# Kernel optimization log

Hardware: AMD Instinct MI355X
Metric: run time of the kernel (lower is better)

## Reference

```python
import jax, jax.numpy as jnp
import numpy as np

BETA = 0.02  # soft-argmax temperature (CATs / matchsplat default)


def _resize_bilinear_ac(x, out_h, out_w):
    """Bilinear resize over the last two dims, align_corners=True (matches F.interpolate)."""
    H, W = x.shape[-2], x.shape[-1]
    ys = jnp.linspace(0.0, H - 1.0, out_h)
    xs = jnp.linspace(0.0, W - 1.0, out_w)
    y0 = jnp.floor(ys).astype(jnp.int32)
    y1 = jnp.minimum(y0 + 1, H - 1)
    x0 = jnp.floor(xs).astype(jnp.int32)
    x1 = jnp.minimum(x0 + 1, W - 1)
    wy = (ys - y0).astype(x.dtype)
    wx = (xs - x0).astype(x.dtype)
    rows = x[..., y0, :] * (1.0 - wy)[:, None] + x[..., y1, :] * wy[:, None]
    return rows[..., x0] * (1.0 - wx) + rows[..., x1] * wx


def _correlation(f0, f1):
    # f0, f1: [B, C, H, W] -> dense 4D cost volume [B, H0, W0, H1, W1], scaled by 1/sqrt(C)
    b, c, h, w = f0.shape
    return jnp.einsum('bchw,bcuv->bhwuv', f0, f1) / (c ** 0.5)


def _interpolate4d(x, size):
    # x: [B, ch, h1, w1, h2, w2]; separable bilinear over (h2,w2) then (h1,w1), align_corners=True
    B, ch, h1, w1, h2, w2 = x.shape
    x = _resize_bilinear_ac(x.reshape(B, ch * h1 * w1, h2, w2), size[2], size[3])
    x = x.reshape(B, ch, h1, w1, size[2], size[3])
    x = jnp.transpose(x, (0, 1, 4, 5, 2, 3)).reshape(B, ch * size[2] * size[3], h1, w1)
    x = _resize_bilinear_ac(x, size[0], size[1])
    x = x.reshape(B, ch, size[2], size[3], size[0], size[1])
    return jnp.transpose(x, (0, 1, 4, 5, 2, 3))


def _soft_argmax(corr):
    # corr: [B, Hs*Ws, Ht, Wt]; softmax over source positions per target pixel,
    # then marginal expectations of normalized [-1,1] coordinates.
    b, c, h, w = corr.shape
    prob = jax.nn.softmax(corr / BETA, axis=1).reshape(b, h, w, h, w)
    x_normal = jnp.linspace(-1.0, 1.0, w, dtype=corr.dtype)
    y_normal = jnp.linspace(-1.0, 1.0, h, dtype=corr.dtype)
    grid_x = (prob.sum(axis=1) * x_normal[None, :, None, None]).sum(axis=1)[:, None]  # [B,1,h,w]
    grid_y = (prob.sum(axis=2) * y_normal[None, :, None, None]).sum(axis=1)[:, None]
    return grid_x, grid_y


def _mapping_to_flow(mapping):
    # mapping: [B,2,H,W] normalized coords in [-1,1] -> pixel-space flow (map - identity grid)
    B, _, H, W = mapping.shape
    mx = (mapping[:, 0] + 1.0) * (W - 1) / 2.0
    my = (mapping[:, 1] + 1.0) * (H - 1) / 2.0
    gx = jnp.arange(W, dtype=mapping.dtype)[None, :]
    gy = jnp.arange(H, dtype=mapping.dtype)[:, None]
    return jnp.stack([mx - gx, my - gy], axis=1)


def _forward(feat0_c, feat1_c, feat0_f, feat1_f):
    B = feat0_c.shape[0]
    S = 64
    corr_c = _correlation(feat0_c, feat1_c)                        # [B,32,32,32,32]
    corr_c = _interpolate4d(corr_c[:, None], (S, S, S, S))[:, 0]   # [B,64,64,64,64]
    corr_f = _correlation(feat0_f, feat1_f)                        # [B,64,64,64,64]
    c = ((corr_c + corr_f) * 0.5)[:, None]                         # [B,1,64,64,64,64]
    c_flip = jnp.transpose(c, (0, 1, 4, 5, 2, 3))
    gx, gy = _soft_argmax(c_flip.reshape(B, S * S, S, S))
    flow = _mapping_to_flow(jnp.concatenate([gx, gy], axis=1))
    gxf, gyf = _soft_argmax(c.reshape(B, S * S, S, S))
    flow_flip = _mapping_to_flow(jnp.concatenate([gxf, gyf], axis=1))
    trans_features = jnp.stack([feat0_f, feat1_f], axis=1)         # [B,2,C,64,64]
    tc = jnp.stack([feat0_c, feat1_c], axis=1)
    C = tc.shape[2]
    tc = _resize_bilinear_ac(tc.reshape(B * 2, C, tc.shape[-2], tc.shape[-1]), S, S)
    trans_features_coarse = tc.reshape(B, 2, C, S, S)
    return trans_features, trans_features_coarse, c, c_flip, flow, flow_flip


def setup_inputs():
    key = jax.random.key(0)
    k0, k1, k2, k3 = jax.random.split(key, 4)
    B, C = 2, 128
    return {
        'feat0_c': jax.random.normal(k0, (B, C, 32, 32), dtype=jnp.float32),
        'feat1_c': jax.random.normal(k1, (B, C, 32, 32), dtype=jnp.float32),
        'feat0_f': jax.random.normal(k2, (B, C, 64, 64), dtype=jnp.float32),
        'feat1_f': jax.random.normal(k3, (B, C, 64, 64), dtype=jnp.float32),
    }


def reference(feat0_c, feat1_c, feat0_f, feat1_f):
    return _forward(feat0_c, feat1_c, feat0_f, feat1_f)
```

## Files before the change

### kernel.cpp

```cpp
#include <hip/hip_runtime.h>
#include <math.h>

#define SCALE_C 0.08838834764831845f
#define INV_BETA 50.0f
#define STEP63 (2.0f / 63.0f)

__device__ __forceinline__ void interp_coef32(int t, int& i0, int& i1, float& w) {
    float s = (float)(t * 31) / 63.0f;
    i0 = (int)floorf(s);
    if (i0 > 31) i0 = 31;
    i1 = i0 + 1;
    if (i1 > 31) i1 = 31;
    w = s - (float)i0;
}

__global__ __launch_bounds__(256) void k_corr_c(const float* __restrict__ f0c,
                                                const float* __restrict__ f1c,
                                                float* __restrict__ ws) {
    __shared__ float As[16][64];
    __shared__ float Bs[16][64];
    const int b = blockIdx.z;
    const int m0 = blockIdx.y * 64, n0 = blockIdx.x * 64;
    const float* A  = f0c + (long long)b * 131072;
    const float* Bp = f1c + (long long)b * 131072;
    const int tid = threadIdx.x;
    const int tx = tid & 15, ty = tid >> 4;
    const int lk = tid >> 4;
    const int lc = (tid & 15) * 4;
    float acc[4][4] = {{0.f}};
    for (int k0 = 0; k0 < 128; k0 += 16) {
        *(float4*)&As[lk][lc] = *(const float4*)&A[(k0 + lk) * 1024 + m0 + lc];
        *(float4*)&Bs[lk][lc] = *(const float4*)&Bp[(k0 + lk) * 1024 + n0 + lc];
        __syncthreads();
#pragma unroll
        for (int kk = 0; kk < 16; ++kk) {
            float4 a4 = *(float4*)&As[kk][ty * 4];
            float4 b4 = *(float4*)&Bs[kk][tx * 4];
            float av[4] = {a4.x, a4.y, a4.z, a4.w};
            float bv[4] = {b4.x, b4.y, b4.z, b4.w};
#pragma unroll
            for (int i = 0; i < 4; ++i)
#pragma unroll
                for (int j = 0; j < 4; ++j)
                    acc[i][j] = fmaf(av[i], bv[j], acc[i][j]);
        }
        __syncthreads();
    }
#pragma unroll
    for (int i = 0; i < 4; ++i) {
        float4 w4 = make_float4(acc[i][0] * SCALE_C, acc[i][1] * SCALE_C,
                                acc[i][2] * SCALE_C, acc[i][3] * SCALE_C);
        *(float4*)&ws[(long long)b * 1048576 + (long long)(m0 + ty * 4 + i) * 1024 + n0 + tx * 4] = w4;
    }
}

__global__ __launch_bounds__(256, 3) void k_fused2(const float* __restrict__ f0f,
                                                   const float* __restrict__ f1f,
                                                   const float* __restrict__ cws,
                                                   float* __restrict__ c_out,
                                                   float* __restrict__ cf_out,
                                                   float* __restrict__ parts) {
    __shared__ __attribute__((aligned(16))) float smem[12800];
    const int TMP2 = 4096;
    const int b = blockIdx.z, by = blockIdx.y, bx = blockIdx.x;
    const int tid = threadIdx.x;
    const int wv = tid >> 6;
    const int tcl = tid & 7;
    const int trl = (tid >> 3) & 7;
    const int tc = tcl + (wv & 1) * 8;
    const int tr = trl + (wv >> 1) * 8;

    {
        const float* Cc = cws + (long long)b * 1048576;
        for (int e = tid; e < 8192; e += 256) {
            int pair = e >> 11, rem = e & 2047;
            int xc0 = rem >> 6, x1 = rem & 63;
            int s0 = pair >> 1, s1 = pair & 1;
            int ya, yb; float wy0; interp_coef32(2 * by + s0, ya, yb, wy0);
            int za, zb; float wy1; interp_coef32(2 * bx + s1, za, zb, wy1);
            int xa, xb; float wx1; interp_coef32(x1, xa, xb, wx1);
            const float* r0 = Cc + (long long)(ya * 32 + xc0) * 1024;
            const float* r1 = Cc + (long long)(yb * 32 + xc0) * 1024;
            float g0 = (r0[za * 32 + xa] * (1.f - wy1) + r0[zb * 32 + xa] * wy1) * (1.f - wy0)
                     + (r1[za * 32 + xa] * (1.f - wy1) + r1[zb * 32 + xa] * wy1) * wy0;
            float g1 = (r0[za * 32 + xb] * (1.f - wy1) + r0[zb * 32 + xb] * wy1) * (1.f - wy0)
                     + (r1[za * 32 + xb] * (1.f - wy1) + r1[zb * 32 + xb] * wy1) * wy0;
            smem[TMP2 + (pair * 32 + xc0) * 68 + x1] = g0 * (1.f - wx1) + g1 * wx1;
        }
    }

    const float* Ag = f0f + (long long)b * 524288 + by * 128;
    const float* Bg = f1f + (long long)b * 524288 + bx * 128;
    float acc[8][8];
#pragma unroll
    for (int i = 0; i < 8; ++i)
#pragma unroll
        for (int j = 0; j < 8; ++j) acc[i][j] = 0.f;

    for (int ks = 0; ks < 8; ++ks) {
        __syncthreads();
        {
            int v0 = tid, v1 = tid + 256;
            *(float4*)&smem[(v0 >> 5) * 128 + (v0 & 31) * 4] =
                *(const float4*)&Ag[(long long)(ks * 16 + (v0 >> 5)) * 4096 + (v0 & 31) * 4];
            *(float4*)&smem[(v1 >> 5) * 128 + (v1 & 31) * 4] =
                *(const float4*)&Ag[(long long)(ks * 16 + (v1 >> 5)) * 4096 + (v1 & 31) * 4];
            *(float4*)&smem[2048 + (v0 >> 5) * 128 + (v0 & 31) * 4] =
                *(const float4*)&Bg[(long long)(ks * 16 + (v0 >> 5)) * 4096 + (v0 & 31) * 4];
            *(float4*)&smem[2048 + (v1 >> 5) * 128 + (v1 & 31) * 4] =
                *(const float4*)&Bg[(long long)(ks * 16 + (v1 >> 5)) * 4096 + (v1 & 31) * 4];
        }
        __syncthreads();
#pragma unroll
        for (int kk = 0; kk < 16; ++kk) {
            float4 a0 = *(float4*)&smem[kk * 128 + tr * 8];
            float4 a1 = *(float4*)&smem[kk * 128 + tr * 8 + 4];
            float4 b0 = *(float4*)&smem[2048 + kk * 128 + tc * 8];
            float4 b1 = *(float4*)&smem[2048 + kk * 128 + tc * 8 + 4];
            float av[8] = {a0.x, a0.y, a0.z, a0.w, a1.x, a1.y, a1.z, a1.w};
            float bv[8] = {b0.x, b0.y, b0.z, b0.w, b1.x, b1.y, b1.z, b1.w};
#pragma unroll
            for (int i = 0; i < 8; ++i)
#pragma unroll
                for (int j = 0; j < 8; ++j)
                    acc[i][j] = fmaf(av[i], bv[j], acc[i][j]);
        }
    }

    const int pair = wv;
    const int x0b = (tr & 7) * 8, x1b = (tc & 7) * 8;
#pragma unroll
    for (int i = 0; i < 8; ++i) {
        int i0, i1; float w0; interp_coef32(x0b + i, i0, i1, w0);
        float4 ua0 = *(float4*)&smem[TMP2 + (pair * 32 + i0) * 68 + x1b];
        float4 ua1 = *(float4*)&smem[TMP2 + (pair * 32 + i0) * 68 + x1b + 4];
        float4 ub0 = *(float4*)&smem[TMP2 + (pair * 32 + i1) * 68 + x1b];
        float4 ub1 = *(float4*)&smem[TMP2 + (pair * 32 + i1) * 68 + x1b + 4];
        float up[8] = {ua0.x * (1.f - w0) + ub0.x * w0, ua0.y * (1.f - w0) + ub0.y * w0,
                       ua0.z * (1.f - w0) + ub0.z * w0, ua0.w * (1.f - w0) + ub0.w * w0,
                       ua1.x * (1.f - w0) + ub1.x * w0, ua1.y * (1.f - w0) + ub1.y * w0,
                       ua1.z * (1.f - w0) + ub1.z * w0, ua1.w * (1.f - w0) + ub1.w * w0};
#pragma unroll
        for (int j = 0; j < 8; ++j)
            acc[i][j] = (acc[i][j] * SCALE_C + up[j]) * 0.5f;
    }

    {
        long long cb = ((long long)b << 24) + (long long)(by * 128 + tr * 8) * 4096 + bx * 128 + tc * 8;
#pragma unroll
        for (int i = 0; i < 8; ++i) {
            *(float4*)&c_out[cb + (long long)i * 4096] =
                make_float4(acc[i][0], acc[i][1], acc[i][2], acc[i][3]);
            *(float4*)&c_out[cb + (long long)i * 4096 + 4] =
                make_float4(acc[i][4], acc[i][5], acc[i][6], acc[i][7]);
        }
        long long fb = ((long long)b << 24) + (long long)(bx * 128 + tc * 8) * 4096 + by * 128 + tr * 8;
#pragma unroll
        for (int j = 0; j < 8; ++j) {
            *(float4*)&cf_out[fb + (long long)j * 4096] =
                make_float4(acc[0][j], acc[1][j], acc[2][j], acc[3][j]);
            *(float4*)&cf_out[fb + (long long)j * 4096 + 4] =
                make_float4(acc[4][j], acc[5][j], acc[6][j], acc[7][j]);
        }
    }

    float4* pred4 = (float4*)smem;
    float4* parts4 = (float4*)parts;
    __syncthreads();

    {
        float yn1 = -1.f + (float)(2 * bx + (tc >> 3)) * STEP63;
#pragma unroll
        for (int i = 0; i < 8; ++i) {
            float m = acc[i][0];
#pragma unroll
            for (int j = 1; j < 8; ++j) m = fmaxf(m, acc[i][j]);
            m = fmaxf(m, __shfl_xor(m, 1, 64));
            m = fmaxf(m, __shfl_xor(m, 2, 64));
            m = fmaxf(m, __shfl_xor(m, 4, 64));
            float l = 0.f, sx = 0.f;
#pragma unroll
            for (int j = 0; j < 8; ++j) {
                float e = __expf((acc[i][j] - m) * INV_BETA);
                l += e;
                sx += e * (-1.f + (float)(x1b + j) * STEP63);
            }
            l += __shfl_xor(l, 1, 64);  sx += __shfl_xor(sx, 1, 64);
            l += __shfl_xor(l, 2, 64);  sx += __shfl_xor(sx, 2, 64);
            l += __shfl_xor(l, 4, 64);  sx += __shfl_xor(sx, 4, 64);
            if (tcl == 0) pred4[(wv & 1) * 128 + tr * 8 + i] = make_float4(m, l, sx, yn1 * l);
        }
    }
    __syncthreads();
    if (tid < 128) {
        float4 h0 = pred4[tid], h1 = pred4[128 + tid];
        float M = fmaxf(h0.x, h1.x);
        float s0 = __expf((h0.x - M) * INV_BETA);
        float s1 = __expf((h1.x - M) * INV_BETA);
        parts4[((long long)b * 4096 + by * 128 + tid) * 32 + bx] =
            make_float4(M, h0.y * s0 + h1.y * s1, h0.z * s0 + h1.z * s1, h0.w * s0 + h1.w * s1);
    }
    __syncthreads();

    {
        float yn0 = -1.f + (float)(2 * by + (tr >> 3)) * STEP63;
#pragma unroll
        for (int j = 0; j < 8; ++j) {
            float m = acc[0][j];
#pragma unroll
            for (int i = 1; i < 8; ++i) m = fmaxf(m, acc[i][j]);
            m = fmaxf(m, __shfl_xor(m, 8, 64));
            m = fmaxf(m, __shfl_xor(m, 16, 64));
            m = fmaxf(m, __shfl_xor(m, 32, 64));
            float l = 0.f, sx = 0.f;
#pragma unroll
            for (int i = 0; i < 8; ++i) {
                float e = __expf((acc[i][j] - m) * INV_BETA);
                l += e;
                sx += e * (-1.f + (float)(x0b + i) * STEP63);
            }
            l += __shfl_xor(l, 8, 64);   sx += __shfl_xor(sx, 8, 64);
            l += __shfl_xor(l, 16, 64);  sx += __shfl_xor(sx, 16, 64);
            l += __shfl_xor(l, 32, 64);  sx += __shfl_xor(sx, 32, 64);
            if (trl == 0) pred4[(wv >> 1) * 128 + tc * 8 + j] = make_float4(m, l, sx, yn0 * l);
        }
    }
    __syncthreads();
    if (tid < 128) {
        float4 h0 = pred4[tid], h1 = pred4[128 + tid];
        float M = fmaxf(h0.x, h1.x);
        float s0 = __expf((h0.x - M) * INV_BETA);
        float s1 = __expf((h1.x - M) * INV_BETA);
        parts4[262144 + ((long long)b * 4096 + bx * 128 + tid) * 32 + by] =
            make_float4(M, h0.y * s0 + h1.y * s1, h0.z * s0 + h1.z * s1, h0.w * s0 + h1.w * s1);
    }
}

__global__ __launch_bounds__(256) void k_flow(const float* __restrict__ parts,
                                              float* __restrict__ flow,
                                              float* __restrict__ flowf) {
    const int row = blockIdx.x * 4 + (threadIdx.x >> 6);
    const int lane = threadIdx.x & 63;
    const float4* p4 = (const float4*)parts + (long long)row * 32;
    float m = -1e30f, l = 0.f, sx = 0.f, sy = 0.f;
    if (lane < 32) { float4 v = p4[lane]; m = v.x; l = v.y; sx = v.z; sy = v.w; }
    float M = m;
#pragma unroll
    for (int off = 1; off < 64; off <<= 1) M = fmaxf(M, __shfl_xor(M, off, 64));
    float s = __expf((m - M) * INV_BETA);
    l *= s; sx *= s; sy *= s;
#pragma unroll
    for (int off = 1; off < 64; off <<= 1) {
        l += __shfl_xor(l, off, 64);
        sx += __shfl_xor(sx, off, 64);
        sy += __shfl_xor(sy, off, 64);
    }
    if (lane == 0) {
        float gx = sx / l, gy = sy / l;
        float mx = (gx + 1.f) * 31.5f, my = (gy + 1.f) * 31.5f;
        int dir = row >> 13, b = (row >> 12) & 1, p = row & 4095;
        float* o = dir ? flowf : flow;
        o[(long long)b * 8192 + p] = mx - (float)(p & 63);
        o[(long long)b * 8192 + 4096 + p] = my - (float)(p >> 6);
    }
}

__global__ void k_copy_trans(const float* __restrict__ f0f, const float* __restrict__ f1f,
                             float* __restrict__ out1) {
    int idx = blockIdx.x * 256 + threadIdx.x;
    int bv = idx >> 17;
    int r = idx & 131071;
    int b = bv >> 1, v = bv & 1;
    const float4* src = (const float4*)(v ? f1f : f0f) + (long long)b * 131072 + r;
    ((float4*)out1)[idx] = *src;
}

__global__ void k_coarse(const float* __restrict__ f0c, const float* __restrict__ f1c,
                         float* __restrict__ out2) {
    int idx = blockIdx.x * 256 + threadIdx.x;
    int x = idx & 63, y = (idx >> 6) & 63, ch = (idx >> 12) & 127;
    int v = (idx >> 19) & 1, b = idx >> 20;
    int iy0, iy1; float wy; interp_coef32(y, iy0, iy1, wy);
    int ix0, ix1; float wx; interp_coef32(x, ix0, ix1, wx);
    const float* src = (v ? f1c : f0c) + (long long)(b * 128 + ch) * 1024;
    float a  = src[iy0 * 32 + ix0] * (1.f - wy) + src[iy1 * 32 + ix0] * wy;
    float c2 = src[iy0 * 32 + ix1] * (1.f - wy) + src[iy1 * 32 + ix1] * wy;
    out2[idx] = a * (1.f - wx) + c2 * wx;
}

__global__ __launch_bounds__(256) void k_fused_fb(const float* __restrict__ f0f,
                                                  const float* __restrict__ f1f,
                                                  const float* __restrict__ cws,
                                                  float* __restrict__ c_out,
                                                  float* __restrict__ cf_out) {
    __shared__ float As[16][64];
    __shared__ float Bs[16][64];
    __shared__ float tmp[32][33];
    const int b = blockIdx.z, y0 = blockIdx.y, y1 = blockIdx.x;
    const int tid = threadIdx.x;
    const int tx = tid & 15, ty = tid >> 4;
    const float* A  = f0f + (long long)b * 524288 + y0 * 64;
    const float* Bp = f1f + (long long)b * 524288 + y1 * 64;
    int iy0a, iy0b; float wy0; interp_coef32(y0, iy0a, iy0b, wy0);
    int iy1a, iy1b; float wy1; interp_coef32(y1, iy1a, iy1b, wy1);
    const float* Cc = cws + (long long)b * 1048576;
    for (int r = tid; r < 1024; r += 256) {
        int i = r >> 5, j = r & 31;
        const float* ra = Cc + (long long)(iy0a * 32 + i) * 1024;
        const float* rb = Cc + (long long)(iy0b * 32 + i) * 1024;
        float va = ra[iy1a * 32 + j] * (1.f - wy1) + ra[iy1b * 32 + j] * wy1;
        float vb = rb[iy1a * 32 + j] * (1.f - wy1) + rb[iy1b * 32 + j] * wy1;
        tmp[i][j] = va * (1.f - wy0) + vb * wy0;
    }
    float acc[4][4] = {{0.f}};
    const int lk = tid >> 4;
    const int lc = (tid & 15) * 4;
    for (int k0 = 0; k0 < 128; k0 += 16) {
        *(float4*)&As[lk][lc] = *(const float4*)&A[(long long)(k0 + lk) * 4096 + lc];
        *(float4*)&Bs[lk][lc] = *(const float4*)&Bp[(long long)(k0 + lk) * 4096 + lc];
        __syncthreads();
#pragma unroll
        for (int kk = 0; kk < 16; ++kk) {
            float4 a4 = *(float4*)&As[kk][ty * 4];
            float4 b4 = *(float4*)&Bs[kk][tx * 4];
            float av[4] = {a4.x, a4.y, a4.z, a4.w};
            float bv[4] = {b4.x, b4.y, b4.z, b4.w};
#pragma unroll
            for (int i = 0; i < 4; ++i)
#pragma unroll
                for (int j = 0; j < 4; ++j)
                    acc[i][j] = fmaf(av[i], bv[j], acc[i][j]);
        }
        __syncthreads();
    }
    int ix0a[4], ix0b[4]; float wx0[4];
    int ix1a[4], ix1b[4]; float wx1[4];
#pragma unroll
    for (int i = 0; i < 4; ++i) interp_coef32(ty * 4 + i, ix0a[i], ix0b[i], wx0[i]);
#pragma unroll
    for (int j = 0; j < 4; ++j) interp_coef32(tx * 4 + j, ix1a[j], ix1b[j], wx1[j]);
    float val[4][4];
#pragma unroll
    for (int i = 0; i < 4; ++i)
#pragma unroll
        for (int j = 0; j < 4; ++j) {
            float ta = tmp[ix0a[i]][ix1a[j]] * (1.f - wx1[j]) + tmp[ix0a[i]][ix1b[j]] * wx1[j];
            float tb = tmp[ix0b[i]][ix1a[j]] * (1.f - wx1[j]) + tmp[ix0b[i]][ix1b[j]] * wx1[j];
            val[i][j] = (acc[i][j] * SCALE_C + (ta * (1.f - wx0[i]) + tb * wx0[i])) * 0.5f;
        }
    const long long cbase = ((long long)b << 24) + (long long)(y0 * 64) * 4096 + y1 * 64;
#pragma unroll
    for (int i = 0; i < 4; ++i)
        *(float4*)&c_out[cbase + (long long)(ty * 4 + i) * 4096 + tx * 4] =
            make_float4(val[i][0], val[i][1], val[i][2], val[i][3]);
    const long long fbase = ((long long)b << 24) + (long long)(y1 * 64) * 4096 + y0 * 64;
#pragma unroll
    for (int j = 0; j < 4; ++j)
        *(float4*)&cf_out[fbase + (long long)(tx * 4 + j) * 4096 + ty * 4] =
            make_float4(val[0][j], val[1][j], val[2][j], val[3][j]);
}

__global__ __launch_bounds__(256) void k_softargmax(const float* __restrict__ cmat,
                                                    float* __restrict__ flow_out) {
    const int tid = threadIdx.x;
    const float4* src = (const float4*)cmat + (long long)blockIdx.x * 1024;
    float4 r0 = src[tid];
    float4 r1 = src[tid + 256];
    float4 r2 = src[tid + 512];
    float4 r3 = src[tid + 768];
    float m = fmaxf(fmaxf(fmaxf(r0.x, r0.y), fmaxf(r0.z, r0.w)),
                    fmaxf(fmaxf(r1.x, r1.y), fmaxf(r1.z, r1.w)));
    m = fmaxf(m, fmaxf(fmaxf(r2.x, r2.y), fmaxf(r2.z, r2.w)));
    m = fmaxf(m, fmaxf(fmaxf(r3.x, r3.y), fmaxf(r3.z, r3.w)));
    __shared__ float red[16];
    const int lane = tid & 63, wave = tid >> 6;
#pragma unroll
    for (int off = 32; off > 0; off >>= 1) m = fmaxf(m, __shfl_xor(m, off, 64));
    if (lane == 0) red[wave] = m;
    __syncthreads();
    m = fmaxf(fmaxf(red[0], red[1]), fmaxf(red[2], red[3]));
    float l = 0.f, sx = 0.f, sy = 0.f;
#pragma unroll
    for (int s = 0; s < 4; ++s) {
        float4 r = (s == 0) ? r0 : (s == 1) ? r1 : (s == 2) ? r2 : r3;
        int f = tid + s * 256;
        float yn = -1.f + (float)(f >> 4) * STEP63;
        float xb = (float)((f & 15) * 4);
        float e0 = __expf((r.x - m) * 50.f);
        float e1 = __expf((r.y - m) * 50.f);
        float e2 = __expf((r.z - m) * 50.f);
        float e3 = __expf((r.w - m) * 50.f);
        float es = e0 + e1 + e2 + e3;
        l += es;
        sy += es * yn;
        sx += e0 * (-1.f + xb * STEP63) + e1 * (-1.f + (xb + 1.f) * STEP63)
            + e2 * (-1.f + (xb + 2.f) * STEP63) + e3 * (-1.f + (xb + 3.f) * STEP63);
    }
#pragma unroll
    for (int off = 32; off > 0; off >>= 1) {
        l  += __shfl_xor(l, off, 64);
        sx += __shfl_xor(sx, off, 64);
        sy += __shfl_xor(sy, off, 64);
    }
    if (lane == 0) { red[4 + wave] = l; red[8 + wave] = sx; red[12 + wave] = sy; }
    __syncthreads();
    if (tid == 0) {
        float L  = red[4] + red[5] + red[6] + red[7];
        float SX = red[8] + red[9] + red[10] + red[11];
        float SY = red[12] + red[13] + red[14] + red[15];
        float mx = (SX / L + 1.f) * 31.5f;
        float my = (SY / L + 1.f) * 31.5f;
        int bi = blockIdx.x;
        int b = bi >> 12, p = bi & 4095;
        flow_out[(long long)b * 8192 + p]        = mx - (float)(p & 63);
        flow_out[(long long)b * 8192 + 4096 + p] = my - (float)(p >> 6);
    }
}

extern "C" void kernel_launch(void* const* d_in, const int* in_sizes, int n_in,
                              void* d_out, int out_size, void* d_ws, size_t ws_size,
                              hipStream_t stream) {
    const float* f0c = (const float*)d_in[0];
    const float* f1c = (const float*)d_in[1];
    const float* f0f = (const float*)d_in[2];
    const float* f1f = (const float*)d_in[3];
    float* out = (float*)d_out;

    float* c_out  = out + 4194304;
    float* cf_out = out + 37748736;
    float* flow   = out + 71303168;
    float* flowf  = out + 71319552;

    if (ws_size >= (size_t)16777216) {
        float* parts = (float*)d_ws;
        float* cws   = parts + 2097152;
        k_corr_c<<<dim3(16, 16, 2), 256, 0, stream>>>(f0c, f1c, cws);
        k_fused2<<<dim3(32, 32, 2), 256, 0, stream>>>(f0f, f1f, cws, c_out, cf_out, parts);
        k_flow<<<4096, 256, 0, stream>>>(parts, flow, flowf);
        k_copy_trans<<<2048, 256, 0, stream>>>(f0f, f1f, out);
        k_coarse<<<8192, 256, 0, stream>>>(f0c, f1c, out + 2097152);
    } else {
        float* corr_ws = out;
        k_corr_c<<<dim3(16, 16, 2), 256, 0, stream>>>(f0c, f1c, corr_ws);
        k_fused_fb<<<dim3(64, 64, 2), 256, 0, stream>>>(f0f, f1f, corr_ws, c_out, cf_out);
        k_copy_trans<<<2048, 256, 0, stream>>>(f0f, f1f, out);
        k_coarse<<<8192, 256, 0, stream>>>(f0c, f1c, out + 2097152);
        k_softargmax<<<8192, 256, 0, stream>>>(c_out, flow);
        k_softargmax<<<8192, 256, 0, stream>>>(cf_out, flowf);
    }
}
```

Before: 454.1 us.

## Use split-bf16 MFMA for fine correlation GEMM with pre-transposed planes

Adds a pre-pass kernel that splits each fp32 fine feature into high and low bf16 parts and transposes them to pixel-major layout, staged in the output buffer before it is overwritten. The fused correlation kernel then computes the 4096x4096 GEMM with three bf16 MFMA products per tile (hi*hi, lo*hi, hi*lo), loading fragments straight from global memory instead of doing fp32 FMA through shared memory. This moves the dominant compute onto matrix cores at the cost of an extra pass over the fine features and some loss of precision from the bf16x3 approximation. The epilogue, upsampling lookup and soft-argmax reductions are remapped to the MFMA accumulator layout.

```diff
diff --git a/kernel.cpp b/kernel.cpp
--- a/kernel.cpp
+++ b/kernel.cpp
@@ -4,6 +4,9 @@
 #define SCALE_C 0.08838834764831845f
 #define INV_BETA 50.0f
 #define STEP63 (2.0f / 63.0f)
+
+typedef short bf16x8 __attribute__((ext_vector_type(8)));
+typedef float f32x4 __attribute__((ext_vector_type(4)));
 
 __device__ __forceinline__ void interp_coef32(int t, int& i0, int& i1, float& w) {
     float s = (float)(t * 31) / 63.0f;
@@ -54,24 +57,68 @@
     }
 }
 
-__global__ __launch_bounds__(256, 3) void k_fused2(const float* __restrict__ f0f,
-                                                   const float* __restrict__ f1f,
+__global__ __launch_bounds__(256) void k_split(const float* __restrict__ f0f,
+                                               const float* __restrict__ f1f,
+                                               unsigned short* __restrict__ hi,
+                                               unsigned short* __restrict__ lo) {
+    __shared__ unsigned int t[64 * 132];
+    const int m = blockIdx.y;
+    const int pt = blockIdx.x;
+    const float* src = ((m >> 1) ? f1f : f0f) + (size_t)(m & 1) * 524288 + pt * 64;
+    const int tid = threadIdx.x;
+#pragma unroll
+    for (int p = 0; p < 8; ++p) {
+        int k = p * 16 + (tid >> 4);
+        int px = (tid & 15) * 4;
+        float4 v = *(const float4*)&src[(size_t)k * 4096 + px];
+        float vv[4] = {v.x, v.y, v.z, v.w};
+#pragma unroll
+        for (int j = 0; j < 4; ++j) {
+            float x = vv[j];
+            unsigned int u = __float_as_uint(x);
+            unsigned int h = (u + 0x7FFFu + ((u >> 16) & 1u)) >> 16;
+            float r = x - __uint_as_float(h << 16);
+            unsigned int ur = __float_as_uint(r);
+            unsigned int l2 = (ur + 0x7FFFu + ((ur >> 16) & 1u)) >> 16;
+            t[(px + j) * 132 + k] = h | (l2 << 16);
+        }
+    }
+    __syncthreads();
+    const int row = tid >> 2, ks = (tid & 3) * 32;
+    size_t obase = ((size_t)m * 4096 + (size_t)pt * 64 + row) * 128 + ks;
+#pragma unroll
+    for (int c = 0; c < 4; ++c) {
+        unsigned int u[8];
+        *(uint4*)&u[0] = *(const uint4*)&t[row * 132 + ks + c * 8];
+        *(uint4*)&u[4] = *(const uint4*)&t[row * 132 + ks + c * 8 + 4];
+        uint4 ho, lw;
+        ho.x = (u[0] & 0xFFFFu) | (u[1] << 16);
+        ho.y = (u[2] & 0xFFFFu) | (u[3] << 16);
+        ho.z = (u[4] & 0xFFFFu) | (u[5] << 16);
+        ho.w = (u[6] & 0xFFFFu) | (u[7] << 16);
+        lw.x = (u[0] >> 16) | (u[1] & 0xFFFF0000u);
+        lw.y = (u[2] >> 16) | (u[3] & 0xFFFF0000u);
+        lw.z = (u[4] >> 16) | (u[5] & 0xFFFF0000u);
+        lw.w = (u[6] >> 16) | (u[7] & 0xFFFF0000u);
+        *(uint4*)&hi[obase + c * 8] = ho;
+        *(uint4*)&lo[obase + c * 8] = lw;
+    }
+}
+
+__global__ __launch_bounds__(256, 3) void k_fused2(const unsigned short* __restrict__ planes,
                                                    const float* __restrict__ cws,
                                                    float* __restrict__ c_out,
                                                    float* __restrict__ cf_out,
                                                    float* __restrict__ parts) {
-    __shared__ __attribute__((aligned(16))) float smem[12800];
-    const int TMP2 = 4096;
+    __shared__ __attribute__((aligned(16))) float smem[8448];
     const int b = blockIdx.z, by = blockIdx.y, bx = blockIdx.x;
     const int tid = threadIdx.x;
-    const int wv = tid >> 6;
-    const int tcl = tid & 7;
-    const int trl = (tid >> 3) & 7;
-    const int tc = tcl + (wv & 1) * 8;
-    const int tr = trl + (wv >> 1) * 8;
+    const int wv = tid >> 6, lane = tid & 63;
+    const int lr = lane & 15, lq = lane >> 4;
+    const int wr = wv >> 1, wc = wv & 1;
 
     {
-        const float* Cc = cws + (long long)b * 1048576;
+        const float* Cc = cws + (size_t)b * 1048576;
         for (int e = tid; e < 8192; e += 256) {
             int pair = e >> 11, rem = e & 2047;
             int xc0 = rem >> 6, x1 = rem & 63;
@@ -79,88 +126,87 @@
             int ya, yb; float wy0; interp_coef32(2 * by + s0, ya, yb, wy0);
             int za, zb; float wy1; interp_coef32(2 * bx + s1, za, zb, wy1);
             int xa, xb; float wx1; interp_coef32(x1, xa, xb, wx1);
-            const float* r0 = Cc + (long long)(ya * 32 + xc0) * 1024;
-            const float* r1 = Cc + (long long)(yb * 32 + xc0) * 1024;
+            const float* r0 = Cc + (size_t)(ya * 32 + xc0) * 1024;
+            const float* r1 = Cc + (size_t)(yb * 32 + xc0) * 1024;
             float g0 = (r0[za * 32 + xa] * (1.f - wy1) + r0[zb * 32 + xa] * wy1) * (1.f - wy0)
                      + (r1[za * 32 + xa] * (1.f - wy1) + r1[zb * 32 + xa] * wy1) * wy0;
             float g1 = (r0[za * 32 + xb] * (1.f - wy1) + r0[zb * 32 + xb] * wy1) * (1.f - wy0)
                      + (r1[za * 32 + xb] * (1.f - wy1) + r1[zb * 32 + xb] * wy1) * wy0;
-            smem[TMP2 + (pair * 32 + xc0) * 68 + x1] = g0 * (1.f - wx1) + g1 * wx1;
-        }
-    }
-
-    const float* Ag = f0f + (long long)b * 524288 + by * 128;
-    const float* Bg = f1f + (long long)b * 524288 + bx * 128;
-    float acc[8][8];
-#pragma unroll
-    for (int i = 0; i < 8; ++i)
-#pragma unroll
-        for (int j = 0; j < 8; ++j) acc[i][j] = 0.f;
-
-    for (int ks = 0; ks < 8; ++ks) {
-        __syncthreads();
-        {
-            int v0 = tid, v1 = tid + 256;
-            *(float4*)&smem[(v0 >> 5) * 128 + (v0 & 31) * 4] =
-                *(const float4*)&Ag[(long long)(ks * 16 + (v0 >> 5)) * 4096 + (v0 & 31) * 4];
-            *(float4*)&smem[(v1 >> 5) * 128 + (v1 & 31) * 4] =
-                *(const float4*)&Ag[(long long)(ks * 16 + (v1 >> 5)) * 4096 + (v1 & 31) * 4];
-            *(float4*)&smem[2048 + (v0 >> 5) * 128 + (v0 & 31) * 4] =
-                *(const float4*)&Bg[(long long)(ks * 16 + (v0 >> 5)) * 4096 + (v0 & 31) * 4];
-            *(float4*)&smem[2048 + (v1 >> 5) * 128 + (v1 & 31) * 4] =
-                *(const float4*)&Bg[(long long)(ks * 16 + (v1 >> 5)) * 4096 + (v1 & 31) * 4];
-        }
-        __syncthreads();
-#pragma unroll
-        for (int kk = 0; kk < 16; ++kk) {
-            float4 a0 = *(float4*)&smem[kk * 128 + tr * 8];
-            float4 a1 = *(float4*)&smem[kk * 128 + tr * 8 + 4];
-            float4 b0 = *(float4*)&smem[2048 + kk * 128 + tc * 8];
-            float4 b1 = *(float4*)&smem[2048 + kk * 128 + tc * 8 + 4];
-            float av[8] = {a0.x, a0.y, a0.z, a0.w, a1.x, a1.y, a1.z, a1.w};
-            float bv[8] = {b0.x, b0.y, b0.z, b0.w, b1.x, b1.y, b1.z, b1.w};
-#pragma unroll
-            for (int i = 0; i < 8; ++i)
-#pragma unroll
-                for (int j = 0; j < 8; ++j)
-                    acc[i][j] = fmaf(av[i], bv[j], acc[i][j]);
-        }
-    }
-
-    const int pair = wv;
-    const int x0b = (tr & 7) * 8, x1b = (tc & 7) * 8;
-#pragma unroll
-    for (int i = 0; i < 8; ++i) {
-        int i0, i1; float w0; interp_coef32(x0b + i, i0, i1, w0);
-        float4 ua0 = *(float4*)&smem[TMP2 + (pair * 32 + i0) * 68 + x1b];
-        float4 ua1 = *(float4*)&smem[TMP2 + (pair * 32 + i0) * 68 + x1b + 4];
-        float4 ub0 = *(float4*)&smem[TMP2 + (pair * 32 + i1) * 68 + x1b];
-        float4 ub1 = *(float4*)&smem[TMP2 + (pair * 32 + i1) * 68 + x1b + 4];
-        float up[8] = {ua0.x * (1.f - w0) + ub0.x * w0, ua0.y * (1.f - w0) + ub0.y * w0,
-                       ua0.z * (1.f - w0) + ub0.z * w0, ua0.w * (1.f - w0) + ub0.w * w0,
-                       ua1.x * (1.f - w0) + ub1.x * w0, ua1.y * (1.f - w0) + ub1.y * w0,
-                       ua1.z * (1.f - w0) + ub1.z * w0, ua1.w * (1.f - w0) + ub1.w * w0};
-#pragma unroll
-        for (int j = 0; j < 8; ++j)
-            acc[i][j] = (acc[i][j] * SCALE_C + up[j]) * 0.5f;
-    }
-
+            smem[(pair * 64 + x1) * 33 + xc0] = g0 * (1.f - wx1) + g1 * wx1;
+        }
+    }
+
+    const unsigned short* Ah = planes + (size_t)b * 524288       + (size_t)(by * 128 + wr * 64) * 128;
+    const unsigned short* Bh = planes + (size_t)(2 + b) * 524288 + (size_t)(bx * 128 + wc * 64) * 128;
+    f32x4 acc[4][4];
+#pragma unroll
+    for (int i = 0; i < 4; ++i)
+#pragma unroll
+        for (int j = 0; j < 4; ++j) acc[i][j] = (f32x4){0.f, 0.f, 0.f, 0.f};
+
+#pragma unroll 1
+    for (int kc = 0; kc < 4; ++kc) {
+        const int ko = kc * 32 + lq * 8;
+        bf16x8 ah[4], al[4], bh[4], bl[4];
+#pragma unroll
+        for (int t = 0; t < 4; ++t) {
+            const unsigned short* pa = Ah + (size_t)(t * 16 + lr) * 128 + ko;
+            const unsigned short* pb = Bh + (size_t)(t * 16 + lr) * 128 + ko;
+            ah[t] = *(const bf16x8*)pa;
+            al[t] = *(const bf16x8*)(pa + 2097152);
+            bh[t] = *(const bf16x8*)pb;
+            bl[t] = *(const bf16x8*)(pb + 2097152);
+        }
+#pragma unroll
+        for (int ni = 0; ni < 4; ++ni)
+#pragma unroll
+            for (int mi = 0; mi < 4; ++mi) {
+                f32x4 a = acc[mi][ni];
+                a = __builtin_amdgcn_mfma_f32_16x16x32_bf16(ah[mi], bh[ni], a, 0, 0, 0);
+                a = __builtin_amdgcn_mfma_f32_16x16x32_bf16(al[mi], bh[ni], a, 0, 0, 0);
+                a = __builtin_amdgcn_mfma_f32_16x16x32_bf16(ah[mi], bl[ni], a, 0, 0, 0);
+                acc[mi][ni] = a;
+            }
+    }
+
+    __syncthreads();
+
+#pragma unroll
+    for (int mi = 0; mi < 4; ++mi)
+#pragma unroll
+        for (int dr = 0; dr < 4; ++dr) {
+            int x0 = mi * 16 + lq * 4 + dr;
+            float s = (float)(x0 * 31) / 63.0f;
+            int i0 = (int)s;
+            float w = s - (float)i0;
+            int i1 = i0 + 1; if (i1 > 31) i1 = 31;
+#pragma unroll
+            for (int ni = 0; ni < 4; ++ni) {
+                const float* t2 = &smem[(wv * 64 + ni * 16 + lr) * 33];
+                float up = t2[i0] * (1.f - w) + t2[i1] * w;
+                acc[mi][ni][dr] = (acc[mi][ni][dr] * SCALE_C + up) * 0.5f;
+            }
+        }
+
+    const int rowbase = by * 128 + wr * 64, colbase = bx * 128 + wc * 64;
     {
-        long long cb = ((long long)b << 24) + (long long)(by * 128 + tr * 8) * 4096 + bx * 128 + tc * 8;
-#pragma unroll
-        for (int i = 0; i < 8; ++i) {
-            *(float4*)&c_out[cb + (long long)i * 4096] =
-                make_float4(acc[i][0], acc[i][1], acc[i][2], acc[i][3]);
-            *(float4*)&c_out[cb + (long long)i * 4096 + 4] =
-                make_float4(acc[i][4], acc[i][5], acc[i][6], acc[i][7]);
-        }
-        long long fb = ((long long)b << 24) + (long long)(bx * 128 + tc * 8) * 4096 + by * 128 + tr * 8;
-#pragma unroll
-        for (int j = 0; j < 8; ++j) {
-            *(float4*)&cf_out[fb + (long long)j * 4096] =
-                make_float4(acc[0][j], acc[1][j], acc[2][j], acc[3][j]);
-            *(float4*)&cf_out[fb + (long long)j * 4096 + 4] =
-                make_float4(acc[4][j], acc[5][j], acc[6][j], acc[7][j]);
+        size_t cb = ((size_t)b << 24) + (size_t)rowbase * 4096 + colbase;
+        size_t fb = ((size_t)b << 24) + (size_t)colbase * 4096 + rowbase;
+#pragma unroll
+        for (int mi = 0; mi < 4; ++mi) {
+#pragma unroll
+            for (int dr = 0; dr < 4; ++dr) {
+                int ro = mi * 16 + lq * 4 + dr;
+#pragma unroll
+                for (int ni = 0; ni < 4; ++ni)
+                    c_out[cb + (size_t)ro * 4096 + ni * 16 + lr] = acc[mi][ni][dr];
+            }
+#pragma unroll
+            for (int ni = 0; ni < 4; ++ni) {
+                int co = ni * 16 + lr;
+                *(float4*)&cf_out[fb + (size_t)co * 4096 + mi * 16 + lq * 4] =
+                    make_float4(acc[mi][ni][0], acc[mi][ni][1], acc[mi][ni][2], acc[mi][ni][3]);
+            }
         }
     }
 
@@ -169,27 +215,31 @@
     __syncthreads();
 
     {
-        float yn1 = -1.f + (float)(2 * bx + (tc >> 3)) * STEP63;
-#pragma unroll
-        for (int i = 0; i < 8; ++i) {
-            float m = acc[i][0];
-#pragma unroll
-            for (int j = 1; j < 8; ++j) m = fmaxf(m, acc[i][j]);
-            m = fmaxf(m, __shfl_xor(m, 1, 64));
-            m = fmaxf(m, __shfl_xor(m, 2, 64));
-            m = fmaxf(m, __shfl_xor(m, 4, 64));
-            float l = 0.f, sx = 0.f;
-#pragma unroll
-            for (int j = 0; j < 8; ++j) {
-                float e = __expf((acc[i][j] - m) * INV_BETA);
-                l += e;
-                sx += e * (-1.f + (float)(x1b + j) * STEP63);
+        float yn1 = -1.f + (float)(2 * bx + wc) * STEP63;
+#pragma unroll
+        for (int mi = 0; mi < 4; ++mi)
+#pragma unroll
+            for (int dr = 0; dr < 4; ++dr) {
+                float m = fmaxf(fmaxf(acc[mi][0][dr], acc[mi][1][dr]),
+                                fmaxf(acc[mi][2][dr], acc[mi][3][dr]));
+                m = fmaxf(m, __shfl_xor(m, 1, 64));
+                m = fmaxf(m, __shfl_xor(m, 2, 64));
+                m = fmaxf(m, __shfl_xor(m, 4, 64));
+                m = fmaxf(m, __shfl_xor(m, 8, 64));
+                float l = 0.f, sx = 0.f;
+#pragma unroll
+                for (int ni = 0; ni < 4; ++ni) {
+                    float e = __expf((acc[mi][ni][dr] - m) * INV_BETA);
+                    l += e;
+                    sx += e * (-1.f + (float)(ni * 16 + lr) * STEP63);
+                }
+                l += __shfl_xor(l, 1, 64);  sx += __shfl_xor(sx, 1, 64);
+                l += __shfl_xor(l, 2, 64);  sx += __shfl_xor(sx, 2, 64);
+                l += __shfl_xor(l, 4, 64);  sx += __shfl_xor(sx, 4, 64);
+                l += __shfl_xor(l, 8, 64);  sx += __shfl_xor(sx, 8, 64);
+                if (lr == 0)
+                    pred4[wc * 128 + wr * 64 + mi * 16 + lq * 4 + dr] = make_float4(m, l, sx, yn1 * l);
             }
-            l += __shfl_xor(l, 1, 64);  sx += __shfl_xor(sx, 1, 64);
-            l += __shfl_xor(l, 2, 64);  sx += __shfl_xor(sx, 2, 64);
-            l += __shfl_xor(l, 4, 64);  sx += __shfl_xor(sx, 4, 64);
-            if (tcl == 0) pred4[(wv & 1) * 128 + tr * 8 + i] = make_float4(m, l, sx, yn1 * l);
-        }
     }
     __syncthreads();
     if (tid < 128) {
@@ -197,32 +247,35 @@
         float M = fmaxf(h0.x, h1.x);
         float s0 = __expf((h0.x - M) * INV_BETA);
         float s1 = __expf((h1.x - M) * INV_BETA);
-        parts4[((long long)b * 4096 + by * 128 + tid) * 32 + bx] =
+        parts4[((size_t)b * 4096 + by * 128 + tid) * 32 + bx] =
             make_float4(M, h0.y * s0 + h1.y * s1, h0.z * s0 + h1.z * s1, h0.w * s0 + h1.w * s1);
     }
     __syncthreads();
 
     {
-        float yn0 = -1.f + (float)(2 * by + (tr >> 3)) * STEP63;
-#pragma unroll
-        for (int j = 0; j < 8; ++j) {
-            float m = acc[0][j];
-#pragma unroll
-            for (int i = 1; i < 8; ++i) m = fmaxf(m, acc[i][j]);
-            m = fmaxf(m, __shfl_xor(m, 8, 64));
+        float yn0 = -1.f + (float)(2 * by + wr) * STEP63;
+#pragma unroll
+        for (int ni = 0; ni < 4; ++ni) {
+            float m = acc[0][ni][0];
+#pragma unroll
+            for (int mi = 0; mi < 4; ++mi)
+#pragma unroll
+                for (int dr = 0; dr < 4; ++dr) m = fmaxf(m, acc[mi][ni][dr]);
             m = fmaxf(m, __shfl_xor(m, 16, 64));
             m = fmaxf(m, __shfl_xor(m, 32, 64));
             float l = 0.f, sx = 0.f;
 #pragma unroll
-            for (int i = 0; i < 8; ++i) {
-                float e = __expf((acc[i][j] - m) * INV_BETA);
-                l += e;
-                sx += e * (-1.f + (float)(x0b + i) * STEP63);
-            }
-            l += __shfl_xor(l, 8, 64);   sx += __shfl_xor(sx, 8, 64);
+            for (int mi = 0; mi < 4; ++mi)
+#pragma unroll
+                for (int dr = 0; dr < 4; ++dr) {
+                    float e = __expf((acc[mi][ni][dr] - m) * INV_BETA);
+                    l += e;
+                    sx += e * (-1.f + (float)(mi * 16 + lq * 4 + dr) * STEP63);
+                }
             l += __shfl_xor(l, 16, 64);  sx += __shfl_xor(sx, 16, 64);
             l += __shfl_xor(l, 32, 64);  sx += __shfl_xor(sx, 32, 64);
-            if (trl == 0) pred4[(wv >> 1) * 128 + tc * 8 + j] = make_float4(m, l, sx, yn0 * l);
+            if (lq == 0)
+                pred4[wr * 128 + wc * 64 + ni * 16 + lr] = make_float4(m, l, sx, yn0 * l);
         }
     }
     __syncthreads();
@@ -231,7 +284,7 @@
         float M = fmaxf(h0.x, h1.x);
         float s0 = __expf((h0.x - M) * INV_BETA);
         float s1 = __expf((h1.x - M) * INV_BETA);
-        parts4[262144 + ((long long)b * 4096 + bx * 128 + tid) * 32 + by] =
+        parts4[262144 + ((size_t)b * 4096 + bx * 128 + tid) * 32 + by] =
             make_float4(M, h0.y * s0 + h1.y * s1, h0.z * s0 + h1.z * s1, h0.w * s0 + h1.w * s1);
     }
 }
@@ -434,8 +487,11 @@
     if (ws_size >= (size_t)16777216) {
         float* parts = (float*)d_ws;
         float* cws   = parts + 2097152;
+        unsigned short* hi = (unsigned short*)out;
+        unsigned short* lo = hi + 2097152;
+        k_split<<<dim3(64, 4, 1), 256, 0, stream>>>(f0f, f1f, hi, lo);
         k_corr_c<<<dim3(16, 16, 2), 256, 0, stream>>>(f0c, f1c, cws);
-        k_fused2<<<dim3(32, 32, 2), 256, 0, stream>>>(f0f, f1f, cws, c_out, cf_out, parts);
+        k_fused2<<<dim3(32, 32, 2), 256, 0, stream>>>(hi, cws, c_out, cf_out, parts);
         k_flow<<<4096, 256, 0, stream>>>(parts, flow, flowf);
         k_copy_trans<<<2048, 256, 0, stream>>>(f0f, f1f, out);
         k_coarse<<<8192, 256, 0, stream>>>(f0c, f1c, out + 2097152);
```

Measured after the change: 430.0 us. 1.06x faster.
